# Kernel tuning notes

Measured on AMD Instinct MI355X. Metric: run time of the kernel, lower is better.

## Reference

```python
import jax, jax.numpy as jnp
import numpy as np

NUM_HEADS = 16
EMB = 1024
V_IN = 512
V_OUT = 1024


def setup_inputs() -> dict:
    key = jax.random.key(0)
    ks = jax.random.split(key, 11)
    s = 0.02
    return {
        "query": jax.random.normal(ks[0], (8, 512, EMB), jnp.float32),
        "key": jax.random.normal(ks[1], (8, 1024, V_IN), jnp.float32),
        "value": jax.random.normal(ks[2], (8, 1024, V_IN), jnp.float32),
        "Wq": jax.random.normal(ks[3], (EMB, EMB), jnp.float32) * s,
        "bq": jax.random.normal(ks[4], (EMB,), jnp.float32) * s,
        "Wk": jax.random.normal(ks[5], (V_IN, EMB), jnp.float32) * s,
        "bk": jax.random.normal(ks[6], (EMB,), jnp.float32) * s,
        "Wv": jax.random.normal(ks[7], (V_IN, V_OUT), jnp.float32) * s,
        "bv": jax.random.normal(ks[8], (V_OUT,), jnp.float32) * s,
        "Wo": jax.random.normal(ks[9], (V_OUT, EMB), jnp.float32) * s,
        "bo": jax.random.normal(ks[10], (EMB,), jnp.float32) * s,
    }


def reference(query, key, value, Wq, bq, Wk, bk, Wv, bv, Wo, bo):
    B, Lq, _ = query.shape
    Lk = key.shape[1]
    H = NUM_HEADS
    dh = EMB // H          # 64, key/query head dim (used as softmax scale)
    dv = V_OUT // H        # 64, value head dim
    q = (query @ Wq + bq).reshape(B, Lq, H, dh)   # [B,Lq,H,dh]
    k = (key @ Wk + bk).reshape(B, Lk, H, dh)     # [B,Lk,H,dh]
    v = (value @ Wv + bv).reshape(B, Lk, H, dv)   # [B,Lk,H,dv]
    scale = 1.0 / np.sqrt(dh).astype(np.float32)
    scores = jnp.einsum('bqhd,bkhd->bhqk', q * scale, k)  # [B,H,Lq,Lk]
    attn = jax.nn.softmax(scores, axis=-1)
    ctx = jnp.einsum('bhqk,bkhd->bqhd', attn, v).reshape(B, Lq, V_OUT)
    return ctx @ Wo + bo  # [B,Lq,EMB]
```

## Files before the change

### kernel.cpp

```cpp
#include <hip/hip_runtime.h>

#define EMB  1024
#define VIN  512
#define VOUT 1024
#define NH   16
#define DH   64
#define BB   8
#define LQ   512
#define LK   1024

typedef __attribute__((ext_vector_type(8))) short bf16x8;
typedef __attribute__((ext_vector_type(4))) float f32x4;

typedef const __attribute__((address_space(1))) unsigned int* gptr_t;
typedef __attribute__((address_space(3))) unsigned int* lptr_t;

__device__ __forceinline__ unsigned short f2bf(float x) {
    unsigned int u = __float_as_uint(x);
    u += 0x7FFF + ((u >> 16) & 1);
    return (unsigned short)(u >> 16);
}
__device__ __forceinline__ float bf2f(unsigned short h) {
    return __uint_as_float(((unsigned int)h) << 16);
}
__device__ __forceinline__ float fexp2(float x) {
    return __builtin_amdgcn_exp2f(x);
}

#define SWZ(row, cb) (((row) << 7) + ((cb) ^ (((row) & 7) << 4)))

__global__ __launch_bounds__(256) void asplit3(const float* __restrict__ q,
                                               const float* __restrict__ k,
                                               const float* __restrict__ v,
                                               unsigned short* __restrict__ Aq,
                                               unsigned short* __restrict__ Ak,
                                               unsigned short* __restrict__ Av)
{
    const int which = blockIdx.x >> 12;
    const float* in = (which == 0) ? q : (which == 1) ? k : v;
    unsigned short* out = (which == 0) ? Aq : (which == 1) ? Ak : Av;
    const int i = (blockIdx.x & 4095) * 256 + threadIdx.x;
    float val[4];
    *reinterpret_cast<float4*>(val) = *reinterpret_cast<const float4*>(&in[(size_t)i * 4]);
    unsigned short h[4];
#pragma unroll
    for (int j = 0; j < 4; ++j) h[j] = f2bf(val[j]);
    *reinterpret_cast<uint2*>(&out[(size_t)i * 4]) = *reinterpret_cast<uint2*>(h);
}

__device__ __forceinline__ void wtile(const float* W, unsigned short* Wht,
                                      unsigned short* Wlt, int K, int N,
                                      int bx, int by, int tx, int ty)
{
    __shared__ float t[32][33];
    const int n0 = bx * 32, k0 = by * 32;
#pragma unroll
    for (int r = 0; r < 32; r += 8)
        t[ty + r][tx] = W[(size_t)(k0 + ty + r) * N + n0 + tx];
    __syncthreads();
#pragma unroll
    for (int r = 0; r < 32; r += 8) {
        float x = t[tx][ty + r];
        unsigned short h = f2bf(x);
        size_t o = (size_t)(n0 + ty + r) * K + k0 + tx;
        Wht[o] = h;
        if (Wlt) Wlt[o] = f2bf(x - bf2f(h));
    }
}

__global__ __launch_bounds__(256) void wsplit_all(const float* __restrict__ Wq,
                                                  const float* __restrict__ Wk,
                                                  const float* __restrict__ Wv,
                                                  const float* __restrict__ Wo,
                                                  unsigned short* __restrict__ Wqt,
                                                  unsigned short* __restrict__ Wkt,
                                                  unsigned short* __restrict__ Wvt,
                                                  unsigned short* __restrict__ Woh,
                                                  unsigned short* __restrict__ Wol)
{
    const int id = blockIdx.x;
    const int tx = threadIdx.x, ty = threadIdx.y;
    if (id < 1024)       wtile(Wq, Wqt, nullptr, 1024, 1024, id & 31, id >> 5, tx, ty);
    else if (id < 1536)  wtile(Wk, Wkt, nullptr, 512, 1024, (id - 1024) & 31, (id - 1024) >> 5, tx, ty);
    else if (id < 2048)  wtile(Wv, Wvt, nullptr, 512, 1024, (id - 1536) & 31, (id - 1536) >> 5, tx, ty);
    else                 wtile(Wo, Woh, Wol, 1024, 1024, (id - 2048) & 31, (id - 2048) >> 5, tx, ty);
}

__device__ __forceinline__ void stagehalf(const unsigned short* g0, int Kstride,
                                          unsigned short* l0, int lane)
{
#pragma unroll
    for (int r = 0; r < 8; ++r) {
        int row  = r * 8 + (lane >> 3);
        int colb = ((lane & 7) << 4) ^ ((row & 7) << 4);
        const unsigned short* src = g0 + (size_t)row * Kstride + (colb >> 1);
        __builtin_amdgcn_global_load_lds((gptr_t)src, (lptr_t)(l0 + r * 512), 16, 0, 0);
    }
}

template<int EPI>
__global__ __launch_bounds__(256, 2) void gemm1(const unsigned short* __restrict__ Ah,
                                                const unsigned short* __restrict__ Bht,
                                                const float* __restrict__ bias,
                                                unsigned short* __restrict__ Ch,
                                                int M, int N, int K)
{
    __shared__ unsigned short As[2][128 * 64], Bs[2][128 * 64];

    const int nbx = N >> 7;
    const int nwg = gridDim.x;
    const int qq  = nwg >> 3;
    const int id  = blockIdx.x;
    const int swz = (id & 7) * qq + (id >> 3);
    const int bx = swz % nbx, by = swz / nbx;
    const int m0 = by * 128, n0 = bx * 128;

    const int tid  = threadIdx.x;
    const int lane = tid & 63;
    const int w    = tid >> 6;
    const int wm = (w & 1) * 64;
    const int wn = (w >> 1) * 64;
    const int lr = lane & 15;
    const int lk = lane >> 4;

    f32x4 acc[4][4];
#pragma unroll
    for (int i = 0; i < 4; ++i)
#pragma unroll
        for (int j = 0; j < 4; ++j) acc[i][j] = (f32x4)(0.f);

    const unsigned short* mysrc = (w < 2)
        ? Ah  + (size_t)(m0 + (w & 1) * 64) * K
        : Bht + (size_t)(n0 + (w & 1) * 64) * K;
    const int lofs = (w & 1) * 4096;
    unsigned short* pl0 = ((w < 2) ? As[0] : Bs[0]) + lofs;
    unsigned short* pl1 = ((w < 2) ? As[1] : Bs[1]) + lofs;

    stagehalf(mysrc, K, pl0, lane);

    const int nt = K >> 6;
    for (int t = 0; t < nt; ++t) {
        __syncthreads();
        if (t + 1 < nt)
            stagehalf(mysrc + ((size_t)(t + 1) << 6), K, ((t & 1) ? pl0 : pl1), lane);

        const char* Ac = (const char*)As[t & 1];
        const char* Bc = (const char*)Bs[t & 1];
#pragma unroll
        for (int ks = 0; ks < 2; ++ks) {
            bf16x8 ah[4], bh[4];
            const int cb = ks * 64 + lk * 16;
#pragma unroll
            for (int f = 0; f < 4; ++f) {
                ah[f] = *reinterpret_cast<const bf16x8*>(Ac + SWZ(wm + f * 16 + lr, cb));
                bh[f] = *reinterpret_cast<const bf16x8*>(Bc + SWZ(wn + f * 16 + lr, cb));
            }
#pragma unroll
            for (int fm = 0; fm < 4; ++fm)
#pragma unroll
                for (int fn = 0; fn < 4; ++fn)
                    acc[fm][fn] = __builtin_amdgcn_mfma_f32_16x16x32_bf16(ah[fm], bh[fn], acc[fm][fn], 0, 0, 0);
        }
    }

#pragma unroll
    for (int fn = 0; fn < 4; ++fn) {
        const int col = n0 + wn + fn * 16 + lr;
        const float bv = bias[col];
#pragma unroll
        for (int fm = 0; fm < 4; ++fm) {
            const int row0 = m0 + wm + fm * 16 + lk * 4;
            if constexpr (EPI == 1) {
#pragma unroll
                for (int r = 0; r < 4; ++r)
                    Ch[(size_t)(row0 + r) * N + col] = f2bf(acc[fm][fn][r] + bv);
            } else if constexpr (EPI == 3) {
#pragma unroll
                for (int r = 0; r < 4; ++r)
                    Ch[(size_t)(row0 + r) * N + col] = f2bf((acc[fm][fn][r] + bv) * 0.18033688011112042f);
            } else {
                unsigned short h4[4];
#pragma unroll
                for (int r = 0; r < 4; ++r)
                    h4[r] = f2bf(acc[fm][fn][r] + bv);
                size_t o = (((size_t)((row0 >> 10) * NH + (col >> 6)) * 64 + (col & 63)) << 10) + (row0 & 1023);
                *reinterpret_cast<uint2*>(&Ch[o]) = *reinterpret_cast<uint2*>(h4);
            }
        }
    }
}

__device__ __forceinline__ void stageplane(const unsigned short* g0, int Kstride,
                                           unsigned short* l0, int lane)
{
#pragma unroll
    for (int r = 0; r < 16; ++r) {
        int row  = r * 8 + (lane >> 3);
        int colb = ((lane & 7) << 4) ^ ((row & 7) << 4);
        const unsigned short* src = g0 + (size_t)row * Kstride + (colb >> 1);
        __builtin_amdgcn_global_load_lds((gptr_t)src, (lptr_t)(l0 + r * 512), 16, 0, 0);
    }
}

__global__ __launch_bounds__(256) void gemm2(const unsigned short* __restrict__ Ah,
                                             const unsigned short* __restrict__ Al,
                                             const unsigned short* __restrict__ Bht,
                                             const unsigned short* __restrict__ Blt,
                                             const float* __restrict__ bias,
                                             float* __restrict__ C,
                                             int M, int N, int K)
{
    __shared__ unsigned short As_h[2][128 * 64], As_l[2][128 * 64];
    __shared__ unsigned short Bs_h[2][128 * 64], Bs_l[2][128 * 64];

    const int nbx = N >> 7;
    const int nwg = gridDim.x;
    const int qq  = nwg >> 3;
    const int id  = blockIdx.x;
    const int swz = (id & 7) * qq + (id >> 3);
    const int bx = swz % nbx, by = swz / nbx;
    const int m0 = by * 128, n0 = bx * 128;

    const int tid  = threadIdx.x;
    const int lane = tid & 63;
    const int w    = tid >> 6;
    const int wm = (w & 1) * 64;
    const int wn = (w >> 1) * 64;
    const int lr = lane & 15;
    const int lk = lane >> 4;

    f32x4 acc[4][4];
#pragma unroll
    for (int i = 0; i < 4; ++i)
#pragma unroll
        for (int j = 0; j < 4; ++j) acc[i][j] = (f32x4)(0.f);

    const unsigned short* mysrc =
        (w == 0) ? Ah + (size_t)m0 * K :
        (w == 1) ? Al + (size_t)m0 * K :
        (w == 2) ? Bht + (size_t)n0 * K :
                   Blt + (size_t)n0 * K;
    unsigned short* pl0 = (w == 0) ? As_h[0] : (w == 1) ? As_l[0] : (w == 2) ? Bs_h[0] : Bs_l[0];
    unsigned short* pl1 = (w == 0) ? As_h[1] : (w == 1) ? As_l[1] : (w == 2) ? Bs_h[1] : Bs_l[1];

    stageplane(mysrc, K, pl0, lane);

    const int nt = K >> 6;
    for (int t = 0; t < nt; ++t) {
        __syncthreads();
        if (t + 1 < nt)
            stageplane(mysrc + ((size_t)(t + 1) << 6), K, ((t & 1) ? pl0 : pl1), lane);

        const char* Ahc = (const char*)As_h[t & 1];
        const char* Alc = (const char*)As_l[t & 1];
        const char* Bhc = (const char*)Bs_h[t & 1];
        const char* Blc = (const char*)Bs_l[t & 1];
#pragma unroll
        for (int ks = 0; ks < 2; ++ks) {
            bf16x8 ah[4], al[4], bh[4], bl[4];
            const int cb = ks * 64 + lk * 16;
#pragma unroll
            for (int f = 0; f < 4; ++f) {
                int rowA = wm + f * 16 + lr;
                ah[f] = *reinterpret_cast<const bf16x8*>(Ahc + SWZ(rowA, cb));
                al[f] = *reinterpret_cast<const bf16x8*>(Alc + SWZ(rowA, cb));
                int rowB = wn + f * 16 + lr;
                bh[f] = *reinterpret_cast<const bf16x8*>(Bhc + SWZ(rowB, cb));
                bl[f] = *reinterpret_cast<const bf16x8*>(Blc + SWZ(rowB, cb));
            }
#pragma unroll
            for (int fm = 0; fm < 4; ++fm)
#pragma unroll
                for (int fn = 0; fn < 4; ++fn) {
                    acc[fm][fn] = __builtin_amdgcn_mfma_f32_16x16x32_bf16(ah[fm], bh[fn], acc[fm][fn], 0, 0, 0);
                    acc[fm][fn] = __builtin_amdgcn_mfma_f32_16x16x32_bf16(ah[fm], bl[fn], acc[fm][fn], 0, 0, 0);
                    acc[fm][fn] = __builtin_amdgcn_mfma_f32_16x16x32_bf16(al[fm], bh[fn], acc[fm][fn], 0, 0, 0);
                }
        }
    }

#pragma unroll
    for (int fn = 0; fn < 4; ++fn) {
        const int col = n0 + wn + fn * 16 + lr;
        const float bv = bias[col];
#pragma unroll
        for (int fm = 0; fm < 4; ++fm) {
            const int row0 = m0 + wm + fm * 16 + lk * 4;
#pragma unroll
            for (int r = 0; r < 4; ++r)
                C[(size_t)(row0 + r) * N + col] = acc[fm][fn][r] + bv;
        }
    }
}

__device__ __forceinline__ void stage32(const unsigned short* g0, unsigned short* l0, int lane)
{
#pragma unroll
    for (int r = 0; r < 4; ++r) {
        int row  = r * 8 + (lane >> 3);
        int colb = ((lane & 7) << 4) ^ ((row & 7) << 4);
        const unsigned short* src = g0 + ((size_t)row << 10) + (colb >> 1);
        __builtin_amdgcn_global_load_lds((gptr_t)src, (lptr_t)(l0 + r * 512), 16, 0, 0);
    }
}

__global__ __launch_bounds__(256, 2) void attn_mfma(const unsigned short* __restrict__ Qh,
                                                    const unsigned short* __restrict__ Kh,
                                                    const unsigned short* __restrict__ Vth,
                                                    unsigned short* __restrict__ Ch,
                                                    unsigned short* __restrict__ Cl)
{
    const int id  = blockIdx.x;
    const int qt  = (id >> 3) & 3;
    const int grp = (id & 7) | ((id >> 5) << 3);
    const int h = grp & 15, b = grp >> 4;

    const int tid  = threadIdx.x;
    const int lane = tid & 63;
    const int w    = tid >> 6;
    const int lr   = lane & 15;
    const int lk   = lane >> 4;

    __shared__ unsigned short KVs[2][2][4096];
    __shared__ unsigned short Ps[4][2048];

    bf16x8 qb[2][2];
#pragma unroll
    for (int qf = 0; qf < 2; ++qf) {
        const unsigned short* qrow =
            &Qh[(size_t)(b * LQ + qt * 128 + w * 32 + qf * 16 + lr) * EMB + h * DH];
        qb[qf][0] = *reinterpret_cast<const bf16x8*>(qrow + lk * 8);
        qb[qf][1] = *reinterpret_cast<const bf16x8*>(qrow + 32 + lk * 8);
    }

    const unsigned short* K0 = Kh + ((size_t)(b * LK) << 10) + h * DH;
    const unsigned short* V0 = Vth + ((size_t)(grp * 64) << 10);

    {
        const int half = (w & 1) * 32;
        if (w < 2) stage32(K0 + ((size_t)half << 10), KVs[0][0] + half * 64, lane);
        else       stage32(V0 + ((size_t)half << 10), KVs[0][1] + half * 64, lane);
    }

    float m[2] = {-1e30f, -1e30f}, lsum[2] = {0.f, 0.f};
    f32x4 acc[2][4];
#pragma unroll
    for (int qf = 0; qf < 2; ++qf)
#pragma unroll
        for (int f = 0; f < 4; ++f) acc[qf][f] = (f32x4)(0.f);

    for (int kt = 0; kt < LK / 64; ++kt) {
        const int cur = kt & 1;
        __syncthreads();

        if (kt + 1 < LK / 64) {
            const size_t koff = (size_t)(kt + 1) * 64;
            const int half = (w & 1) * 32;
            if (w < 2) stage32(K0 + ((koff + half) << 10), KVs[cur ^ 1][0] + half * 64, lane);
            else       stage32(V0 + ((size_t)half << 10) + koff, KVs[cur ^ 1][1] + half * 64, lane);
        }

        const char* Ks = (const char*)KVs[cur][0];
        const char* Vs = (const char*)KVs[cur][1];

        f32x4 s[2][4];
#pragma unroll
        for (int qf = 0; qf < 2; ++qf)
#pragma unroll
            for (int fn = 0; fn < 4; ++fn) s[qf][fn] = (f32x4)(0.f);
#pragma unroll
        for (int ks = 0; ks < 2; ++ks) {
            const int cb = ks * 64 + lk * 16;
#pragma unroll
            for (int fn = 0; fn < 4; ++fn) {
                bf16x8 kb = *reinterpret_cast<const bf16x8*>(Ks + SWZ(fn * 16 + lr, cb));
                s[0][fn] = __builtin_amdgcn_mfma_f32_16x16x32_bf16(kb, qb[0][ks], s[0][fn], 0, 0, 0);
                s[1][fn] = __builtin_amdgcn_mfma_f32_16x16x32_bf16(kb, qb[1][ks], s[1][fn], 0, 0, 0);
            }
        }

#pragma unroll
        for (int qf = 0; qf < 2; ++qf) {
            f32x4 t4 = s[qf][0];
#pragma unroll
            for (int fn = 1; fn < 4; ++fn)
#pragma unroll
                for (int r = 0; r < 4; ++r) t4[r] = fmaxf(t4[r], s[qf][fn][r]);
            float mx = fmaxf(fmaxf(t4[0], t4[1]), fmaxf(t4[2], t4[3]));
            mx = fmaxf(mx, __shfl_xor(mx, 16));
            mx = fmaxf(mx, __shfl_xor(mx, 32));
            float mnew = fmaxf(m[qf], mx);
            float corr = fexp2(m[qf] - mnew);
            m[qf] = mnew;
            float rs = 0.f;
#pragma unroll
            for (int fn = 0; fn < 4; ++fn)
#pragma unroll
                for (int r = 0; r < 4; ++r) {
                    float p = fexp2(s[qf][fn][r] - mnew);
                    s[qf][fn][r] = p;
                    rs += p;
                }
            rs += __shfl_xor(rs, 16);
            rs += __shfl_xor(rs, 32);
            lsum[qf] = lsum[qf] * corr + rs;
#pragma unroll
            for (int f = 0; f < 4; ++f)
#pragma unroll
                for (int r = 0; r < 4; ++r) acc[qf][f][r] *= corr;
        }

#pragma unroll
        for (int qf = 0; qf < 2; ++qf)
#pragma unroll
            for (int fn = 0; fn < 4; ++fn) {
                uint2 pk;
                pk.x = (unsigned int)f2bf(s[qf][fn][0]) | ((unsigned int)f2bf(s[qf][fn][1]) << 16);
                pk.y = (unsigned int)f2bf(s[qf][fn][2]) | ((unsigned int)f2bf(s[qf][fn][3]) << 16);
                *reinterpret_cast<uint2*>((char*)Ps[w] + SWZ(qf * 16 + lr, fn * 32 + lk * 8)) = pk;
            }

#pragma unroll
        for (int ks = 0; ks < 2; ++ks) {
            const int cb = ks * 64 + lk * 16;
            bf16x8 pa0 = *reinterpret_cast<const bf16x8*>((char*)Ps[w] + SWZ(lr, cb));
            bf16x8 pa1 = *reinterpret_cast<const bf16x8*>((char*)Ps[w] + SWZ(16 + lr, cb));
#pragma unroll
            for (int f = 0; f < 4; ++f) {
                bf16x8 vb = *reinterpret_cast<const bf16x8*>(Vs + SWZ(f * 16 + lr, cb));
                acc[0][f] = __builtin_amdgcn_mfma_f32_16x16x32_bf16(vb, pa0, acc[0][f], 0, 0, 0);
                acc[1][f] = __builtin_amdgcn_mfma_f32_16x16x32_bf16(vb, pa1, acc[1][f], 0, 0, 0);
            }
        }
    }

#pragma unroll
    for (int qf = 0; qf < 2; ++qf) {
        float inv = 1.f / lsum[qf];
        const size_t row = (size_t)(b * LQ + qt * 128 + w * 32 + qf * 16 + lr);
#pragma unroll
        for (int f = 0; f < 4; ++f)
#pragma unroll
            for (int r = 0; r < 4; ++r) {
                float x = acc[qf][f][r] * inv;
                unsigned short hh = f2bf(x);
                size_t o = (row << 10) + h * DH + f * 16 + lk * 4 + r;
                Ch[o] = hh;
                Cl[o] = f2bf(x - bf2f(hh));
            }
    }
}

extern "C" void kernel_launch(void* const* d_in, const int* in_sizes, int n_in,
                              void* d_out, int out_size, void* d_ws, size_t ws_size,
                              hipStream_t stream)
{
    const float* query = (const float*)d_in[0];
    const float* key   = (const float*)d_in[1];
    const float* value = (const float*)d_in[2];
    const float* Wq = (const float*)d_in[3];
    const float* bq = (const float*)d_in[4];
    const float* Wk = (const float*)d_in[5];
    const float* bk = (const float*)d_in[6];
    const float* Wv = (const float*)d_in[7];
    const float* bv = (const float*)d_in[8];
    const float* Wo = (const float*)d_in[9];
    const float* bo = (const float*)d_in[10];
    float* out = (float*)d_out;

    unsigned short* Qh  = (unsigned short*)d_ws;
    unsigned short* Kh  = Qh  + (size_t)4194304;
    unsigned short* Vth = Kh  + (size_t)8388608;
    unsigned short* Aq  = Vth + (size_t)8388608;
    unsigned short* Ak  = Aq  + (size_t)4194304;
    unsigned short* Av  = Ak  + (size_t)4194304;
    unsigned short* Ch  = Av  + (size_t)4194304;
    unsigned short* Cl  = Ch  + (size_t)4194304;
    unsigned short* Wqt = Cl  + (size_t)4194304;
    unsigned short* Wkt = Wqt + (size_t)1048576;
    unsigned short* Wvt = Wkt + (size_t)524288;
    unsigned short* Woh = Wvt + (size_t)524288;
    unsigned short* Wol = Woh + (size_t)1048576;

    asplit3<<<12288, 256, 0, stream>>>(query, key, value, Aq, Ak, Av);
    wsplit_all<<<3072, dim3(32, 8), 0, stream>>>(Wq, Wk, Wv, Wo, Wqt, Wkt, Wvt, Woh, Wol);

    gemm1<3><<<(EMB / 128) * (BB * LQ / 128), 256, 0, stream>>>(Aq, Wqt, bq, Qh, BB * LQ, EMB, EMB);
    gemm1<1><<<(EMB / 128) * (BB * LK / 128), 256, 0, stream>>>(Ak, Wkt, bk, Kh, BB * LK, EMB, VIN);
    gemm1<2><<<(VOUT / 128) * (BB * LK / 128), 256, 0, stream>>>(Av, Wvt, bv, Vth, BB * LK, VOUT, VIN);

    attn_mfma<<<LQ / 128 * NH * BB, 256, 0, stream>>>(Qh, Kh, Vth, Ch, Cl);

    gemm2<<<(EMB / 128) * (BB * LQ / 128), 256, 0, stream>>>(Ch, Cl, Woh, Wol, bo, out, BB * LQ, EMB, VOUT);
}
```

Baseline: 138.2 us.

## Load K/V tiles directly into registers with double-buffered prefetch, drop LDS staging

The attention kernel no longer stages K and V tiles through shared memory with global_load_lds and block-wide barriers. Each wave now loads its own MFMA operand fragments for K and V straight from global memory into registers, ping-ponging between two register sets so the next tile's load overlaps the current tile's compute. This removes the __syncthreads per tile and the LDS traffic for K/V. In exchange every wave fetches the full K/V tile separately (4x redundant global/L2 reads) and register pressure rises considerably, which may hurt occupancy under launch_bounds(256,2).

Measured after the change: 156.0 us. 1.13x slower.

```diff
diff --git a/kernel.cpp b/kernel.cpp
--- a/kernel.cpp
+++ b/kernel.cpp
@@ -293,14 +293,91 @@
     }
 }
 
-__device__ __forceinline__ void stage32(const unsigned short* g0, unsigned short* l0, int lane)
-{
-#pragma unroll
-    for (int r = 0; r < 4; ++r) {
-        int row  = r * 8 + (lane >> 3);
-        int colb = ((lane & 7) << 4) ^ ((row & 7) << 4);
-        const unsigned short* src = g0 + ((size_t)row << 10) + (colb >> 1);
-        __builtin_amdgcn_global_load_lds((gptr_t)src, (lptr_t)(l0 + r * 512), 16, 0, 0);
+__device__ __forceinline__ void attn_loadkv(bf16x8 (&KR)[8], bf16x8 (&VR)[8],
+                                            const unsigned short* Kb,
+                                            const unsigned short* Vb,
+                                            int koff, int lr, int lk)
+{
+#pragma unroll
+    for (int ks = 0; ks < 2; ++ks)
+#pragma unroll
+        for (int fn = 0; fn < 4; ++fn) {
+            KR[ks * 4 + fn] = *reinterpret_cast<const bf16x8*>(
+                Kb + (size_t)(koff + fn * 16 + lr) * 1024 + ks * 32 + lk * 8);
+            VR[ks * 4 + fn] = *reinterpret_cast<const bf16x8*>(
+                Vb + (size_t)(fn * 16 + lr) * 1024 + koff + ks * 32 + lk * 8);
+        }
+}
+
+__device__ __forceinline__ void attn_tile(const bf16x8 (&KR)[8], const bf16x8 (&VR)[8],
+                                          const bf16x8 (&qb)[2][2], f32x4 (&acc)[2][4],
+                                          float (&m)[2], float (&lsum)[2],
+                                          char* Psw, int lr, int lk)
+{
+    f32x4 s[2][4];
+#pragma unroll
+    for (int qf = 0; qf < 2; ++qf)
+#pragma unroll
+        for (int fn = 0; fn < 4; ++fn) s[qf][fn] = (f32x4)(0.f);
+#pragma unroll
+    for (int ks = 0; ks < 2; ++ks)
+#pragma unroll
+        for (int fn = 0; fn < 4; ++fn) {
+            s[0][fn] = __builtin_amdgcn_mfma_f32_16x16x32_bf16(KR[ks * 4 + fn], qb[0][ks], s[0][fn], 0, 0, 0);
+            s[1][fn] = __builtin_amdgcn_mfma_f32_16x16x32_bf16(KR[ks * 4 + fn], qb[1][ks], s[1][fn], 0, 0, 0);
+        }
+
+#pragma unroll
+    for (int qf = 0; qf < 2; ++qf) {
+        f32x4 t4 = s[qf][0];
+#pragma unroll
+        for (int fn = 1; fn < 4; ++fn)
+#pragma unroll
+            for (int r = 0; r < 4; ++r) t4[r] = fmaxf(t4[r], s[qf][fn][r]);
+        float mx = fmaxf(fmaxf(t4[0], t4[1]), fmaxf(t4[2], t4[3]));
+        mx = fmaxf(mx, __shfl_xor(mx, 16));
+        mx = fmaxf(mx, __shfl_xor(mx, 32));
+        float mnew = fmaxf(m[qf], mx);
+        float corr = fexp2(m[qf] - mnew);
+        m[qf] = mnew;
+        float rs = 0.f;
+#pragma unroll
+        for (int fn = 0; fn < 4; ++fn)
+#pragma unroll
+            for (int r = 0; r < 4; ++r) {
+                float p = fexp2(s[qf][fn][r] - mnew);
+                s[qf][fn][r] = p;
+                rs += p;
+            }
+        rs += __shfl_xor(rs, 16);
+        rs += __shfl_xor(rs, 32);
+        lsum[qf] = lsum[qf] * corr + rs;
+#pragma unroll
+        for (int f = 0; f < 4; ++f)
+#pragma unroll
+            for (int r = 0; r < 4; ++r) acc[qf][f][r] *= corr;
+    }
+
+#pragma unroll
+    for (int qf = 0; qf < 2; ++qf)
+#pragma unroll
+        for (int fn = 0; fn < 4; ++fn) {
+            uint2 pk;
+            pk.x = (unsigned int)f2bf(s[qf][fn][0]) | ((unsigned int)f2bf(s[qf][fn][1]) << 16);
+            pk.y = (unsigned int)f2bf(s[qf][fn][2]) | ((unsigned int)f2bf(s[qf][fn][3]) << 16);
+            *reinterpret_cast<uint2*>(Psw + SWZ(qf * 16 + lr, fn * 32 + lk * 8)) = pk;
+        }
+
+#pragma unroll
+    for (int ks = 0; ks < 2; ++ks) {
+        const int cb = ks * 64 + lk * 16;
+        bf16x8 pa0 = *reinterpret_cast<const bf16x8*>(Psw + SWZ(lr, cb));
+        bf16x8 pa1 = *reinterpret_cast<const bf16x8*>(Psw + SWZ(16 + lr, cb));
+#pragma unroll
+        for (int f = 0; f < 4; ++f) {
+            acc[0][f] = __builtin_amdgcn_mfma_f32_16x16x32_bf16(VR[ks * 4 + f], pa0, acc[0][f], 0, 0, 0);
+            acc[1][f] = __builtin_amdgcn_mfma_f32_16x16x32_bf16(VR[ks * 4 + f], pa1, acc[1][f], 0, 0, 0);
+        }
     }
 }
 
@@ -321,8 +398,8 @@
     const int lr   = lane & 15;
     const int lk   = lane >> 4;
 
-    __shared__ unsigned short KVs[2][2][4096];
     __shared__ unsigned short Ps[4][2048];
+    char* Psw = (char*)Ps[w];
 
     bf16x8 qb[2][2];
 #pragma unroll
@@ -333,14 +410,8 @@
         qb[qf][1] = *reinterpret_cast<const bf16x8*>(qrow + 32 + lk * 8);
     }
 
-    const unsigned short* K0 = Kh + ((size_t)(b * LK) << 10) + h * DH;
-    const unsigned short* V0 = Vth + ((size_t)(grp * 64) << 10);
-
-    {
-        const int half = (w & 1) * 32;
-        if (w < 2) stage32(K0 + ((size_t)half << 10), KVs[0][0] + half * 64, lane);
-        else       stage32(V0 + ((size_t)half << 10), KVs[0][1] + half * 64, lane);
-    }
+    const unsigned short* Kb = Kh + ((size_t)(b * LK) << 10) + h * DH;
+    const unsigned short* Vb = Vth + ((size_t)(grp * 64) << 10);
 
     float m[2] = {-1e30f, -1e30f}, lsum[2] = {0.f, 0.f};
     f32x4 acc[2][4];
@@ -349,89 +420,15 @@
 #pragma unroll
         for (int f = 0; f < 4; ++f) acc[qf][f] = (f32x4)(0.f);
 
-    for (int kt = 0; kt < LK / 64; ++kt) {
-        const int cur = kt & 1;
-        __syncthreads();
-
-        if (kt + 1 < LK / 64) {
-            const size_t koff = (size_t)(kt + 1) * 64;
-            const int half = (w & 1) * 32;
-            if (w < 2) stage32(K0 + ((koff + half) << 10), KVs[cur ^ 1][0] + half * 64, lane);
-            else       stage32(V0 + ((size_t)half << 10) + koff, KVs[cur ^ 1][1] + half * 64, lane);
-        }
-
-        const char* Ks = (const char*)KVs[cur][0];
-        const char* Vs = (const char*)KVs[cur][1];
-
-        f32x4 s[2][4];
-#pragma unroll
-        for (int qf = 0; qf < 2; ++qf)
-#pragma unroll
-            for (int fn = 0; fn < 4; ++fn) s[qf][fn] = (f32x4)(0.f);
-#pragma unroll
-        for (int ks = 0; ks < 2; ++ks) {
-            const int cb = ks * 64 + lk * 16;
-#pragma unroll
-            for (int fn = 0; fn < 4; ++fn) {
-                bf16x8 kb = *reinterpret_cast<const bf16x8*>(Ks + SWZ(fn * 16 + lr, cb));
-                s[0][fn] = __builtin_amdgcn_mfma_f32_16x16x32_bf16(kb, qb[0][ks], s[0][fn], 0, 0, 0);
-                s[1][fn] = __builtin_amdgcn_mfma_f32_16x16x32_bf16(kb, qb[1][ks], s[1][fn], 0, 0, 0);
-            }
-        }
-
-#pragma unroll
-        for (int qf = 0; qf < 2; ++qf) {
-            f32x4 t4 = s[qf][0];
-#pragma unroll
-            for (int fn = 1; fn < 4; ++fn)
-#pragma unroll
-                for (int r = 0; r < 4; ++r) t4[r] = fmaxf(t4[r], s[qf][fn][r]);
-            float mx = fmaxf(fmaxf(t4[0], t4[1]), fmaxf(t4[2], t4[3]));
-            mx = fmaxf(mx, __shfl_xor(mx, 16));
-            mx = fmaxf(mx, __shfl_xor(mx, 32));
-            float mnew = fmaxf(m[qf], mx);
-            float corr = fexp2(m[qf] - mnew);
-            m[qf] = mnew;
-            float rs = 0.f;
-#pragma unroll
-            for (int fn = 0; fn < 4; ++fn)
-#pragma unroll
-                for (int r = 0; r < 4; ++r) {
-                    float p = fexp2(s[qf][fn][r] - mnew);
-                    s[qf][fn][r] = p;
-                    rs += p;
-                }
-            rs += __shfl_xor(rs, 16);
-            rs += __shfl_xor(rs, 32);
-            lsum[qf] = lsum[qf] * corr + rs;
-#pragma unroll
-            for (int f = 0; f < 4; ++f)
-#pragma unroll
-                for (int r = 0; r < 4; ++r) acc[qf][f][r] *= corr;
-        }
-
-#pragma unroll
-        for (int qf = 0; qf < 2; ++qf)
-#pragma unroll
-            for (int fn = 0; fn < 4; ++fn) {
-                uint2 pk;
-                pk.x = (unsigned int)f2bf(s[qf][fn][0]) | ((unsigned int)f2bf(s[qf][fn][1]) << 16);
-                pk.y = (unsigned int)f2bf(s[qf][fn][2]) | ((unsigned int)f2bf(s[qf][fn][3]) << 16);
-                *reinterpret_cast<uint2*>((char*)Ps[w] + SWZ(qf * 16 + lr, fn * 32 + lk * 8)) = pk;
-            }
-
-#pragma unroll
-        for (int ks = 0; ks < 2; ++ks) {
-            const int cb = ks * 64 + lk * 16;
-            bf16x8 pa0 = *reinterpret_cast<const bf16x8*>((char*)Ps[w] + SWZ(lr, cb));
-            bf16x8 pa1 = *reinterpret_cast<const bf16x8*>((char*)Ps[w] + SWZ(16 + lr, cb));
-#pragma unroll
-            for (int f = 0; f < 4; ++f) {
-                bf16x8 vb = *reinterpret_cast<const bf16x8*>(Vs + SWZ(f * 16 + lr, cb));
-                acc[0][f] = __builtin_amdgcn_mfma_f32_16x16x32_bf16(vb, pa0, acc[0][f], 0, 0, 0);
-                acc[1][f] = __builtin_amdgcn_mfma_f32_16x16x32_bf16(vb, pa1, acc[1][f], 0, 0, 0);
-            }
-        }
+    bf16x8 KA[8], VA[8], KB[8], VB[8];
+    attn_loadkv(KA, VA, Kb, Vb, 0, lr, lk);
+
+    for (int kt = 0; kt < LK / 64; kt += 2) {
+        attn_loadkv(KB, VB, Kb, Vb, (kt + 1) * 64, lr, lk);
+        attn_tile(KA, VA, qb, acc, m, lsum, Psw, lr, lk);
+        if (kt + 2 < LK / 64)
+            attn_loadkv(KA, VA, Kb, Vb, (kt + 2) * 64, lr, lk);
+        attn_tile(KB, VB, qb, acc, m, lsum, Psw, lr, lk);
     }
 
 #pragma unroll
```
